# Optimization experiments

Measured on AMD Instinct MI355X. Metric: run time of the kernel, lower is better.

The kernel has to match this reference:

```python
import jax, jax.numpy as jnp
import numpy as np

N = 200000      # num entities
D_IN = 256      # input_dim
D_OUT = 256     # output_dim
R = 8           # num_relations
E = 150000      # edges per relation


def _xavier(key, shape):
    fan_in, fan_out = shape[-2], shape[-1]
    bound = (6.0 / (fan_in + fan_out)) ** 0.5
    return jax.random.uniform(key, shape, jnp.float32, -bound, bound)


def setup_inputs() -> dict:
    key = jax.random.key(0)
    ks = jax.random.split(key, 5)
    entity_embeddings = jax.random.normal(ks[0], (N, D_IN), jnp.float32)
    relation_weights = _xavier(ks[1], (R, D_IN, D_OUT))
    self_weight = _xavier(ks[2], (D_IN, D_OUT))
    bias_param = jnp.zeros((R, D_OUT), jnp.float32)
    edge_index = jax.random.randint(ks[3], (R, 2, E), 0, N)  # row0=src, row1=tgt
    edge_weights = jax.random.uniform(ks[4], (R, E), jnp.float32)
    return {
        "entity_embeddings": entity_embeddings,
        "relation_weights": relation_weights,
        "self_weight": self_weight,
        "bias_param": bias_param,
        "edge_index": edge_index,
        "edge_weights": edge_weights,
    }


def reference(entity_embeddings, relation_weights, self_weight, bias_param, edge_index, edge_weights):
    num_entities = entity_embeddings.shape[0]
    d_out = relation_weights.shape[2]

    def per_relation(out, inp):
        ei, ew, W, b = inp
        src, tgt = ei[0], ei[1]
        # gather -> per-relation matmul -> edge-weight scale
        msg = (entity_embeddings[src] @ W) * ew[:, None]          # [E, d_out]
        out = out.at[tgt].add(msg)                                 # scatter-add
        # bias added once per unique target node of this relation
        presence = jnp.zeros((num_entities,), entity_embeddings.dtype).at[tgt].set(1.0)
        out = out + presence[:, None] * b
        return out, None

    out0 = jnp.zeros((num_entities, d_out), entity_embeddings.dtype)
    out, _ = jax.lax.scan(per_relation, out0, (edge_index, edge_weights, relation_weights, bias_param))
    return out + entity_embeddings @ self_weight
```

## Files before the change

### kernel.cpp

```cpp
#include <hip/hip_runtime.h>


#define N_ENT 200000
#define D 256
#define R_REL 8
#define E_EDGE 150000
#define TOT_E (R_REL * E_EDGE)
#define MKEY (N_ENT * R_REL)
#define SCAN_B 1024
#define NBLK_SCAN ((MKEY + SCAN_B - 1) / SCAN_B)

typedef __bf16 bf16x8 __attribute__((ext_vector_type(8)));
typedef unsigned short u16x8 __attribute__((ext_vector_type(8)));
typedef float f32x4 __attribute__((ext_vector_type(4)));

__device__ __forceinline__ unsigned short f2bf(float f) {
  unsigned int u = __builtin_bit_cast(unsigned int, f);
  u += 0x7FFFu + ((u >> 16) & 1u);
  return (unsigned short)(u >> 16);
}
__device__ __forceinline__ float bf2f(unsigned short u) {
  return __builtin_bit_cast(float, ((unsigned)u) << 16);
}
__device__ __forceinline__ f32x4 mfma16(u16x8 a, u16x8 b, f32x4 c) {
  return __builtin_amdgcn_mfma_f32_16x16x32_bf16(
      __builtin_bit_cast(bf16x8, a), __builtin_bit_cast(bf16x8, b), c, 0, 0, 0);
}

__global__ __launch_bounds__(256) void k_cvt_x(const float* __restrict__ x,
                                               unsigned short* __restrict__ xh,
                                               const int* __restrict__ ei,
                                               unsigned* __restrict__ counts) {
  int i = blockIdx.x * 256 + threadIdx.x;
  const float4* xv = (const float4*)x;
  float4 a = xv[2 * i], b = xv[2 * i + 1];
  uint4 o;
  o.x = (unsigned)f2bf(a.x) | ((unsigned)f2bf(a.y) << 16);
  o.y = (unsigned)f2bf(a.z) | ((unsigned)f2bf(a.w) << 16);
  o.z = (unsigned)f2bf(b.x) | ((unsigned)f2bf(b.y) << 16);
  o.w = (unsigned)f2bf(b.z) | ((unsigned)f2bf(b.w) << 16);
  ((uint4*)xh)[i] = o;
  if (i < TOT_E) {
    int r = i / E_EDGE, e = i - r * E_EDGE;
    int tgt = ei[(r * 2 + 1) * E_EDGE + e];
    atomicAdd(&counts[r * N_ENT + tgt], 1u);
  }
}

__global__ __launch_bounds__(256) void k_cvt_w(const float* __restrict__ relw,
                                               const float* __restrict__ selfw,
                                               const float* __restrict__ bias,
                                               unsigned short* __restrict__ wf,
                                               unsigned short* __restrict__ bb) {
  if (blockIdx.x < 288) {
    int t = blockIdx.x * 256 + threadIdx.x;
    int rel = t >> 13;
    int rem = t & 8191;
    int kb = rem >> 10;
    int nb = (rem >> 6) & 15;
    int lane = rem & 63;
    const float* W = (rel < R_REL) ? (relw + rel * D * D) : selfw;
    int k0 = kb * 32 + (lane >> 4) * 8;
    int n = nb * 16 + (lane & 15);
    unsigned int o[4];
#pragma unroll
    for (int jj = 0; jj < 4; ++jj) {
      unsigned lo = f2bf(W[(k0 + 2 * jj) * D + n]);
      unsigned hi = f2bf(W[(k0 + 2 * jj + 1) * D + n]);
      o[jj] = lo | (hi << 16);
    }
    ((uint4*)wf)[t] = make_uint4(o[0], o[1], o[2], o[3]);
  } else {
    int t = (blockIdx.x - 288) * 256 + threadIdx.x;
    int nb = t >> 6, lane = t & 63;
    int lk = lane >> 4, n = nb * 16 + (lane & 15);
    unsigned int o[4];
#pragma unroll
    for (int jj = 0; jj < 4; ++jj) {
      unsigned lo = 0, hi = 0;
      if (lk == 0) {
        lo = f2bf(bias[(2 * jj) * D + n]);
        hi = f2bf(bias[(2 * jj + 1) * D + n]);
      }
      o[jj] = lo | (hi << 16);
    }
    ((uint4*)bb)[t] = make_uint4(o[0], o[1], o[2], o[3]);
  }
}

__global__ __launch_bounds__(256) void k_scan1(const unsigned* __restrict__ cnt,
                                               unsigned* __restrict__ off,
                                               unsigned* __restrict__ aux) {
  __shared__ unsigned sc[256];
  int tid = threadIdx.x;
  int base = blockIdx.x * SCAN_B + tid * 4;
  unsigned v[4];
#pragma unroll
  for (int j = 0; j < 4; ++j) v[j] = (base + j < MKEY) ? cnt[base + j] : 0u;
  unsigned s = v[0] + v[1] + v[2] + v[3];
  sc[tid] = s;
  __syncthreads();
  for (int o = 1; o < 256; o <<= 1) {
    unsigned t = (tid >= o) ? sc[tid - o] : 0u;
    __syncthreads();
    sc[tid] += t;
    __syncthreads();
  }
  unsigned excl = sc[tid] - s;
  if (tid == 255) aux[blockIdx.x] = sc[255];
#pragma unroll
  for (int j = 0; j < 4; ++j) {
    if (base + j < MKEY) off[base + j] = excl;
    excl += v[j];
  }
}

__global__ __launch_bounds__(256) void k_scan2(unsigned* __restrict__ aux) {
  __shared__ unsigned sc[256];
  int tid = threadIdx.x;
  int base = tid * 7;
  unsigned v[7];
#pragma unroll
  for (int j = 0; j < 7; ++j) v[j] = (base + j < NBLK_SCAN) ? aux[base + j] : 0u;
  unsigned s = 0;
#pragma unroll
  for (int j = 0; j < 7; ++j) s += v[j];
  sc[tid] = s;
  __syncthreads();
  for (int o = 1; o < 256; o <<= 1) {
    unsigned t = (tid >= o) ? sc[tid - o] : 0u;
    __syncthreads();
    sc[tid] += t;
    __syncthreads();
  }
  unsigned excl = sc[tid] - s;
#pragma unroll
  for (int j = 0; j < 7; ++j) {
    if (base + j < NBLK_SCAN) aux[base + j] = excl;
    excl += v[j];
  }
}

__global__ __launch_bounds__(256) void k_scan3(unsigned* __restrict__ off,
                                               const unsigned* __restrict__ aux) {
  unsigned add = aux[blockIdx.x];
  int base = blockIdx.x * SCAN_B + threadIdx.x * 4;
  if (base + 3 < MKEY) {
    uint4* p = (uint4*)(off + base);
    uint4 x = *p;
    x.x += add; x.y += add; x.z += add; x.w += add;
    *p = x;
  } else {
    for (int j = 0; j < 4; ++j)
      if (base + j < MKEY) off[base + j] += add;
  }
}

__global__ __launch_bounds__(256) void k_scatter(const int* __restrict__ ei,
                                                 const float* __restrict__ ew,
                                                 unsigned* __restrict__ off,
                                                 unsigned* __restrict__ spack,
                                                 float* __restrict__ sewt) {
  int t = blockIdx.x * 256 + threadIdx.x;
  if (t >= TOT_E) return;
  int r = t / E_EDGE, e = t - r * E_EDGE;
  int tgt = ei[(r * 2 + 1) * E_EDGE + e];
  int src = ei[(r * 2) * E_EDGE + e];
  float w = ew[t];
  unsigned pos = atomicAdd(&off[r * N_ENT + tgt], 1u);
  spack[pos] = (unsigned)src | ((unsigned)(tgt & 63) << 18);
  sewt[pos] = w;
}

__device__ __forceinline__ void agg_issue(int g0, int lane, unsigned s0, unsigned e0,
                                          unsigned pkc, float wtc,
                                          const unsigned short* __restrict__ xh,
                                          unsigned char* nxt,
                                          unsigned pk8[8], float wt8[8], ushort4 xv[8]) {
#pragma unroll
  for (int k = 0; k < 8; ++k) {
    int g = g0 + k;
    int wb = (g * 512 + lane * 8) ^ ((g & 7) << 4);
    *(uint2*)(nxt + wb) = make_uint2(0u, 0u);
  }
  int total = (int)(e0 - s0);
  int m0 = total < 8 ? total : 8;
#pragma unroll
  for (int u = 0; u < 8; ++u) {
    pk8[u] = (unsigned)__shfl((int)pkc, u);
    wt8[u] = __shfl(wtc, u);
  }
#pragma unroll
  for (int u = 0; u < 8; ++u) {
    unsigned srcu = (u < m0) ? (pk8[u] & 0x3FFFFu) : 0u;
    xv[u] = *(const ushort4*)(xh + (size_t)srcu * 256 + lane * 4);
  }
}

__device__ __forceinline__ void agg_finish(int lane, unsigned s0, unsigned e0,
                                           unsigned pkc, float wtc,
                                           const unsigned* __restrict__ spack,
                                           const float* __restrict__ sewt,
                                           const unsigned short* __restrict__ xh,
                                           unsigned char* nxt,
                                           const unsigned pk8[8], const float wt8[8],
                                           const ushort4 xv[8]) {
  int total = (int)(e0 - s0);
  if (total <= 0) return;
  int gp = -1;
  float a0 = 0.f, a1 = 0.f, a2 = 0.f, a3 = 0.f;
#define AGG_FLUSH() do { \
    unsigned lo_ = (unsigned)f2bf(a0) | ((unsigned)f2bf(a1) << 16); \
    unsigned hi_ = (unsigned)f2bf(a2) | ((unsigned)f2bf(a3) << 16); \
    int wb_ = (gp * 512 + lane * 8) ^ ((gp & 7) << 4); \
    *(uint2*)(nxt + wb_) = make_uint2(lo_, hi_); } while (0)

  int mch = total < 64 ? total : 64;
  int m0 = mch < 8 ? mch : 8;
#pragma unroll
  for (int u = 0; u < 8; ++u) {
    if (u < m0) {
      int g = (int)(pk8[u] >> 18);
      if (g != gp) {
        if (gp >= 0) AGG_FLUSH();
        a0 = a1 = a2 = a3 = 0.f;
        gp = g;
      }
      float wt = wt8[u];
      a0 += wt * bf2f(xv[u].x);
      a1 += wt * bf2f(xv[u].y);
      a2 += wt * bf2f(xv[u].z);
      a3 += wt * bf2f(xv[u].w);
    }
  }
  for (int g8 = 8; g8 < mch; g8 += 8) {
    unsigned q8[8];
    float v8[8];
#pragma unroll
    for (int u = 0; u < 8; ++u) {
      q8[u] = (unsigned)__shfl((int)pkc, g8 + u);
      v8[u] = __shfl(wtc, g8 + u);
    }
    ushort4 yv[8];
#pragma unroll
    for (int u = 0; u < 8; ++u) {
      unsigned srcu = (g8 + u < mch) ? (q8[u] & 0x3FFFFu) : 0u;
      yv[u] = *(const ushort4*)(xh + (size_t)srcu * 256 + lane * 4);
    }
#pragma unroll
    for (int u = 0; u < 8; ++u) {
      if (g8 + u < mch) {
        int g = (int)(q8[u] >> 18);
        if (g != gp) {
          if (gp >= 0) AGG_FLUSH();
          a0 = a1 = a2 = a3 = 0.f;
          gp = g;
        }
        float wt = v8[u];
        a0 += wt * bf2f(yv[u].x);
        a1 += wt * bf2f(yv[u].y);
        a2 += wt * bf2f(yv[u].z);
        a3 += wt * bf2f(yv[u].w);
      }
    }
  }
  for (unsigned chunk = s0 + 64u; chunk < e0; chunk += 64u) {
    unsigned idx = chunk + (unsigned)lane;
    if (idx >= (unsigned)TOT_E) idx = (unsigned)(TOT_E - 1);
    unsigned pkv = spack[idx];
    float wtv = sewt[idx];
    int rem = (int)(e0 - chunk);
    int m = rem < 64 ? rem : 64;
    for (int g8 = 0; g8 < m; g8 += 8) {
      unsigned q8[8];
      float v8[8];
#pragma unroll
      for (int u = 0; u < 8; ++u) {
        q8[u] = (unsigned)__shfl((int)pkv, g8 + u);
        v8[u] = __shfl(wtv, g8 + u);
      }
      ushort4 yv[8];
#pragma unroll
      for (int u = 0; u < 8; ++u) {
        unsigned srcu = (g8 + u < m) ? (q8[u] & 0x3FFFFu) : 0u;
        yv[u] = *(const ushort4*)(xh + (size_t)srcu * 256 + lane * 4);
      }
#pragma unroll
      for (int u = 0; u < 8; ++u) {
        if (g8 + u < m) {
          int g = (int)(q8[u] >> 18);
          if (g != gp) {
            if (gp >= 0) AGG_FLUSH();
            a0 = a1 = a2 = a3 = 0.f;
            gp = g;
          }
          float wt = v8[u];
          a0 += wt * bf2f(yv[u].x);
          a1 += wt * bf2f(yv[u].y);
          a2 += wt * bf2f(yv[u].z);
          a3 += wt * bf2f(yv[u].w);
        }
      }
    }
  }
  if (gp >= 0) AGG_FLUSH();
#undef AGG_FLUSH
}

__global__ __launch_bounds__(512, 2) void k_main(const unsigned short* __restrict__ xh,
                                                 const unsigned short* __restrict__ wf,
                                                 const unsigned short* __restrict__ bbf,
                                                 const unsigned* __restrict__ counts,
                                                 const unsigned* __restrict__ off_end,
                                                 const unsigned* __restrict__ spack,
                                                 const float* __restrict__ sewt,
                                                 float* __restrict__ out) {
  __shared__ __align__(16) unsigned char As[2 * 32768];
  int n0 = blockIdx.x * 64;
  int tid = threadIdx.x;
  int w = tid >> 6, lane = tid & 63;
  int lm = lane & 15, lk = lane >> 4;
  int rbase = (w >> 2) * 32;
  int cbase = (w & 3) * 4;
  int g0 = w * 8;

  unsigned sB[8], eE[8];
#pragma unroll
  for (int r = 0; r < 8; ++r) {
    int kb2 = r * N_ENT + n0 + w * 8;
    sB[r] = kb2 ? off_end[kb2 - 1] : 0u;
    eE[r] = off_end[kb2 + 7];
  }

  f32x4 acc[2][4] = {};

  {
    const unsigned short* wfb = wf + 8 * 65536;
#pragma unroll
    for (int kb = 0; kb < 8; ++kb) {
      u16x8 a[2], b[4];
#pragma unroll
      for (int mi = 0; mi < 2; ++mi)
        a[mi] = *(const u16x8*)(xh + (size_t)(n0 + rbase + mi * 16 + lm) * 256 + kb * 32 + lk * 8);
#pragma unroll
      for (int ni = 0; ni < 4; ++ni)
        b[ni] = *(const u16x8*)(wfb + ((kb * 16 + cbase + ni) * 64 + lane) * 8);
#pragma unroll
      for (int mi = 0; mi < 2; ++mi)
#pragma unroll
        for (int ni = 0; ni < 4; ++ni)
          acc[mi][ni] = mfma16(a[mi], b[ni], acc[mi][ni]);
    }
  }

  unsigned pk0[8];
  float wt0[8];
#pragma unroll
  for (int r = 0; r < 8; ++r) {
    unsigned idx = sB[r] + (unsigned)lane;
    if (idx >= (unsigned)TOT_E) idx = (unsigned)(TOT_E - 1);
    pk0[r] = spack[idx];
    wt0[r] = sewt[idx];
  }

  {
    unsigned pk8[8];
    float wt8[8];
    ushort4 xv[8];
    agg_issue(g0, lane, sB[0], eE[0], pk0[0], wt0[0], xh, As, pk8, wt8, xv);
    agg_finish(lane, sB[0], eE[0], pk0[0], wt0[0], spack, sewt, xh, As, pk8, wt8, xv);
  }
  __syncthreads();

#pragma unroll
  for (int r = 0; r < 8; ++r) {
    unsigned char* cur = As + (r & 1) * 32768;
    unsigned char* nxt = As + ((r + 1) & 1) * 32768;
    unsigned pk8[8];
    float wt8[8];
    ushort4 xv[8];
    if (r < 7)
      agg_issue(g0, lane, sB[r + 1], eE[r + 1], pk0[r + 1], wt0[r + 1], xh, nxt, pk8, wt8, xv);

    const unsigned short* wfb = wf + r * 65536;
#pragma unroll
    for (int kb = 0; kb < 8; ++kb) {
      u16x8 a[2], b[4];
#pragma unroll
      for (int mi = 0; mi < 2; ++mi) {
        int row = rbase + mi * 16 + lm;
        int byt = (row * 512 + kb * 64 + lk * 16) ^ ((row & 7) << 4);
        a[mi] = *(const u16x8*)(cur + byt);
      }
#pragma unroll
      for (int ni = 0; ni < 4; ++ni)
        b[ni] = *(const u16x8*)(wfb + ((kb * 16 + cbase + ni) * 64 + lane) * 8);
#pragma unroll
      for (int mi = 0; mi < 2; ++mi)
#pragma unroll
        for (int ni = 0; ni < 4; ++ni)
          acc[mi][ni] = mfma16(a[mi], b[ni], acc[mi][ni]);
    }

    if (r < 7)
      agg_finish(lane, sB[r + 1], eE[r + 1], pk0[r + 1], wt0[r + 1], spack, sewt, xh, nxt,
                 pk8, wt8, xv);
    __syncthreads();
  }

  {
    u16x8 bb[4];
#pragma unroll
    for (int ni = 0; ni < 4; ++ni)
      bb[ni] = *(const u16x8*)(bbf + ((cbase + ni) * 64 + lane) * 8);
#pragma unroll
    for (int mi = 0; mi < 2; ++mi) {
      u16x8 pa = {};
      if (lk == 0) {
        int n = n0 + rbase + mi * 16 + lm;
#pragma unroll
        for (int r = 0; r < 8; ++r)
          pa[r] = counts[r * N_ENT + n] ? 0x3F80 : 0;
      }
#pragma unroll
      for (int ni = 0; ni < 4; ++ni)
        acc[mi][ni] = mfma16(pa, bb[ni], acc[mi][ni]);
    }
  }

#pragma unroll
  for (int mi = 0; mi < 2; ++mi)
#pragma unroll
    for (int ni = 0; ni < 4; ++ni) {
      int col = (w & 3) * 64 + ni * 16 + lm;
#pragma unroll
      for (int j = 0; j < 4; ++j) {
        int row = n0 + rbase + mi * 16 + lk * 4 + j;
        out[row * 256 + col] = acc[mi][ni][j];
      }
    }
}

extern "C" void kernel_launch(void* const* d_in, const int* in_sizes, int n_in,
                              void* d_out, int out_size, void* d_ws, size_t ws_size,
                              hipStream_t stream) {
  const float* x = (const float*)d_in[0];
  const float* relw = (const float*)d_in[1];
  const float* selfw = (const float*)d_in[2];
  const float* bias = (const float*)d_in[3];
  const int* ei = (const int*)d_in[4];
  const float* ew = (const float*)d_in[5];
  float* out = (float*)d_out;

  char* ws = (char*)d_ws;
  unsigned short* xh = (unsigned short*)ws;
  unsigned short* wf = (unsigned short*)(ws + 102400000);
  unsigned short* bbf = (unsigned short*)(ws + 103579648);
  unsigned* counts = (unsigned*)(ws + 103596032);
  unsigned* offs = (unsigned*)(ws + 109996032);
  unsigned* aux = (unsigned*)(ws + 116396032);
  unsigned* spack = (unsigned*)(ws + 116404224);
  float* sewt = (float*)(ws + 121204224);

  hipMemsetAsync(counts, 0, (size_t)MKEY * 4, stream);
  k_cvt_x<<<(N_ENT * D) / 2048, 256, 0, stream>>>(x, xh, ei, counts);
  k_cvt_w<<<292, 256, 0, stream>>>(relw, selfw, bias, wf, bbf);
  k_scan1<<<NBLK_SCAN, 256, 0, stream>>>(counts, offs, aux);
  k_scan2<<<1, 256, 0, stream>>>(aux);
  k_scan3<<<NBLK_SCAN, 256, 0, stream>>>(offs, aux);
  k_scatter<<<(TOT_E + 255) / 256, 256, 0, stream>>>(ei, ew, offs, spack, sewt);
  k_main<<<N_ENT / 64, 512, 0, stream>>>(xh, wf, bbf, counts, offs, spack, sewt, out);
}
```

Measured before the change: 747.7 us.

## Aggregate two relations per stage into a single 64KB LDS tile

Replaces the per-relation double-buffered aggregation tile with a single 64x512 bf16 tile holding two relations side by side, so each stage runs a K=512 MFMA loop over two relation weights. The gathers for the next pair are issued before the MFMA loop, but the scatter into LDS now happens after a barrier, so it is no longer overlapped with compute. This halves the number of pipeline stages and barriers per block. Launch bounds are raised to 4 blocks per SM, which tightens register limits and may cause spills, since 16 gathered vectors are now held in flight.

```diff
diff --git a/kernel.cpp b/kernel.cpp
--- a/kernel.cpp
+++ b/kernel.cpp
@@ -172,61 +172,57 @@
   sewt[pos] = w;
 }
 
-__device__ __forceinline__ void agg_issue(int g0, int lane, unsigned s0, unsigned e0,
-                                          unsigned pkc, float wtc,
-                                          const unsigned short* __restrict__ xh,
-                                          unsigned char* nxt,
-                                          unsigned pk8[8], float wt8[8], ushort4 xv[8]) {
-#pragma unroll
-  for (int k = 0; k < 8; ++k) {
-    int g = g0 + k;
-    int wb = (g * 512 + lane * 8) ^ ((g & 7) << 4);
-    *(uint2*)(nxt + wb) = make_uint2(0u, 0u);
-  }
-  int total = (int)(e0 - s0);
-  int m0 = total < 8 ? total : 8;
+__device__ __forceinline__ void agg2_issue(int lane,
+                                           unsigned sLo, unsigned eLo, unsigned pkcLo,
+                                           unsigned sHi, unsigned eHi, unsigned pkcHi,
+                                           const unsigned short* __restrict__ xh,
+                                           ushort4 xv[16]) {
+  int mLo = (int)(eLo - sLo); mLo = mLo < 8 ? mLo : 8;
+  int mHi = (int)(eHi - sHi); mHi = mHi < 8 ? mHi : 8;
 #pragma unroll
   for (int u = 0; u < 8; ++u) {
-    pk8[u] = (unsigned)__shfl((int)pkc, u);
-    wt8[u] = __shfl(wtc, u);
+    unsigned pk = (unsigned)__shfl((int)pkcLo, u);
+    unsigned srcu = (u < mLo) ? (pk & 0x3FFFFu) : 0u;
+    xv[u] = *(const ushort4*)(xh + (size_t)srcu * 256 + lane * 4);
   }
 #pragma unroll
   for (int u = 0; u < 8; ++u) {
-    unsigned srcu = (u < m0) ? (pk8[u] & 0x3FFFFu) : 0u;
-    xv[u] = *(const ushort4*)(xh + (size_t)srcu * 256 + lane * 4);
-  }
-}
-
-__device__ __forceinline__ void agg_finish(int lane, unsigned s0, unsigned e0,
-                                           unsigned pkc, float wtc,
-                                           const unsigned* __restrict__ spack,
-                                           const float* __restrict__ sewt,
-                                           const unsigned short* __restrict__ xh,
-                                           unsigned char* nxt,
-                                           const unsigned pk8[8], const float wt8[8],
-                                           const ushort4 xv[8]) {
+    unsigned pk = (unsigned)__shfl((int)pkcHi, u);
+    unsigned srcu = (u < mHi) ? (pk & 0x3FFFFu) : 0u;
+    xv[8 + u] = *(const ushort4*)(xh + (size_t)srcu * 256 + lane * 4);
+  }
+}
+
+__device__ __forceinline__ void agg_fin_half(int lane, unsigned s0, unsigned e0,
+                                             unsigned pkc, float wtc,
+                                             const unsigned* __restrict__ spack,
+                                             const float* __restrict__ sewt,
+                                             const unsigned short* __restrict__ xh,
+                                             unsigned char* As, int halfOff,
+                                             const ushort4* xv) {
   int total = (int)(e0 - s0);
   if (total <= 0) return;
   int gp = -1;
   float a0 = 0.f, a1 = 0.f, a2 = 0.f, a3 = 0.f;
-#define AGG_FLUSH() do { \
+#define AGG_FLUSH2() do { \
     unsigned lo_ = (unsigned)f2bf(a0) | ((unsigned)f2bf(a1) << 16); \
     unsigned hi_ = (unsigned)f2bf(a2) | ((unsigned)f2bf(a3) << 16); \
-    int wb_ = (gp * 512 + lane * 8) ^ ((gp & 7) << 4); \
-    *(uint2*)(nxt + wb_) = make_uint2(lo_, hi_); } while (0)
+    int wb_ = (gp * 1024 + halfOff + lane * 8) ^ ((gp & 7) << 4); \
+    *(uint2*)(As + wb_) = make_uint2(lo_, hi_); } while (0)
 
   int mch = total < 64 ? total : 64;
   int m0 = mch < 8 ? mch : 8;
 #pragma unroll
   for (int u = 0; u < 8; ++u) {
     if (u < m0) {
-      int g = (int)(pk8[u] >> 18);
+      unsigned pk = (unsigned)__shfl((int)pkc, u);
+      float wt = __shfl(wtc, u);
+      int g = (int)(pk >> 18);
       if (g != gp) {
-        if (gp >= 0) AGG_FLUSH();
+        if (gp >= 0) AGG_FLUSH2();
         a0 = a1 = a2 = a3 = 0.f;
         gp = g;
       }
-      float wt = wt8[u];
       a0 += wt * bf2f(xv[u].x);
       a1 += wt * bf2f(xv[u].y);
       a2 += wt * bf2f(xv[u].z);
@@ -252,7 +248,7 @@
       if (g8 + u < mch) {
         int g = (int)(q8[u] >> 18);
         if (g != gp) {
-          if (gp >= 0) AGG_FLUSH();
+          if (gp >= 0) AGG_FLUSH2();
           a0 = a1 = a2 = a3 = 0.f;
           gp = g;
         }
@@ -290,7 +286,7 @@
         if (g8 + u < m) {
           int g = (int)(q8[u] >> 18);
           if (g != gp) {
-            if (gp >= 0) AGG_FLUSH();
+            if (gp >= 0) AGG_FLUSH2();
             a0 = a1 = a2 = a3 = 0.f;
             gp = g;
           }
@@ -303,11 +299,11 @@
       }
     }
   }
-  if (gp >= 0) AGG_FLUSH();
-#undef AGG_FLUSH
-}
-
-__global__ __launch_bounds__(512, 2) void k_main(const unsigned short* __restrict__ xh,
+  if (gp >= 0) AGG_FLUSH2();
+#undef AGG_FLUSH2
+}
+
+__global__ __launch_bounds__(512, 4) void k_main(const unsigned short* __restrict__ xh,
                                                  const unsigned short* __restrict__ wf,
                                                  const unsigned short* __restrict__ bbf,
                                                  const unsigned* __restrict__ counts,
@@ -315,7 +311,7 @@
                                                  const unsigned* __restrict__ spack,
                                                  const float* __restrict__ sewt,
                                                  float* __restrict__ out) {
-  __shared__ __align__(16) unsigned char As[2 * 32768];
+  __shared__ __align__(16) unsigned char As[64 * 1024];
   int n0 = blockIdx.x * 64;
   int tid = threadIdx.x;
   int w = tid >> 6, lane = tid & 63;
@@ -363,34 +359,41 @@
     wt0[r] = sewt[idx];
   }
 
+  f32x4 z4 = {0.f, 0.f, 0.f, 0.f};
+
   {
-    unsigned pk8[8];
-    float wt8[8];
-    ushort4 xv[8];
-    agg_issue(g0, lane, sB[0], eE[0], pk0[0], wt0[0], xh, As, pk8, wt8, xv);
-    agg_finish(lane, sB[0], eE[0], pk0[0], wt0[0], spack, sewt, xh, As, pk8, wt8, xv);
+    ushort4 xv[16];
+    agg2_issue(lane, sB[0], eE[0], pk0[0], sB[1], eE[1], pk0[1], xh, xv);
+#pragma unroll
+    for (int k = 0; k < 8; ++k) {
+      int g = g0 + k;
+      int wb = (g * 1024 + lane * 16) ^ ((g & 7) << 4);
+      *(f32x4*)(As + wb) = z4;
+    }
+    agg_fin_half(lane, sB[0], eE[0], pk0[0], wt0[0], spack, sewt, xh, As, 0, xv);
+    agg_fin_half(lane, sB[1], eE[1], pk0[1], wt0[1], spack, sewt, xh, As, 512, xv + 8);
   }
   __syncthreads();
 
 #pragma unroll
-  for (int r = 0; r < 8; ++r) {
-    unsigned char* cur = As + (r & 1) * 32768;
-    unsigned char* nxt = As + ((r + 1) & 1) * 32768;
-    unsigned pk8[8];
-    float wt8[8];
-    ushort4 xv[8];
-    if (r < 7)
-      agg_issue(g0, lane, sB[r + 1], eE[r + 1], pk0[r + 1], wt0[r + 1], xh, nxt, pk8, wt8, xv);
-
-    const unsigned short* wfb = wf + r * 65536;
-#pragma unroll
-    for (int kb = 0; kb < 8; ++kb) {
+  for (int p = 0; p < 4; ++p) {
+    ushort4 xv[16];
+    if (p < 3)
+      agg2_issue(lane, sB[2 * p + 2], eE[2 * p + 2], pk0[2 * p + 2],
+                 sB[2 * p + 3], eE[2 * p + 3], pk0[2 * p + 3], xh, xv);
+
+    const unsigned short* wfbL = wf + (2 * p) * 65536;
+    const unsigned short* wfbR = wf + (2 * p + 1) * 65536;
+#pragma unroll
+    for (int kb2 = 0; kb2 < 16; ++kb2) {
+      const unsigned short* wfb = (kb2 < 8) ? wfbL : wfbR;
+      int kb = kb2 & 7;
       u16x8 a[2], b[4];
 #pragma unroll
       for (int mi = 0; mi < 2; ++mi) {
         int row = rbase + mi * 16 + lm;
-        int byt = (row * 512 + kb * 64 + lk * 16) ^ ((row & 7) << 4);
-        a[mi] = *(const u16x8*)(cur + byt);
+        int byt = (row * 1024 + kb2 * 64 + lk * 16) ^ ((row & 7) << 4);
+        a[mi] = *(const u16x8*)(As + byt);
       }
 #pragma unroll
       for (int ni = 0; ni < 4; ++ni)
@@ -402,10 +405,20 @@
           acc[mi][ni] = mfma16(a[mi], b[ni], acc[mi][ni]);
     }
 
-    if (r < 7)
-      agg_finish(lane, sB[r + 1], eE[r + 1], pk0[r + 1], wt0[r + 1], spack, sewt, xh, nxt,
-                 pk8, wt8, xv);
-    __syncthreads();
+    if (p < 3) {
+      __syncthreads();
+#pragma unroll
+      for (int k = 0; k < 8; ++k) {
+        int g = g0 + k;
+        int wb = (g * 1024 + lane * 16) ^ ((g & 7) << 4);
+        *(f32x4*)(As + wb) = z4;
+      }
+      agg_fin_half(lane, sB[2 * p + 2], eE[2 * p + 2], pk0[2 * p + 2], wt0[2 * p + 2],
+                   spack, sewt, xh, As, 0, xv);
+      agg_fin_half(lane, sB[2 * p + 3], eE[2 * p + 3], pk0[2 * p + 3], wt0[2 * p + 3],
+                   spack, sewt, xh, As, 512, xv + 8);
+      __syncthreads();
+    }
   }
 
   {
```

New measurement: 1.001 ms. 1.34x slower.
